# Kernel tuning notes

Measured on AMD Instinct MI355X. Metric: run time of the kernel, lower is better.

The kernel has to match this reference:

```python
import jax, jax.numpy as jnp
import numpy as np

DIM = 1024
N_HEADS = 16
HEAD_DIM = DIM // N_HEADS


def setup_inputs() -> dict:
    key = jax.random.key(0)
    k_x, k_wqkv, k_bqkv, k_wp, k_bp = jax.random.split(key, 5)
    s = 1.0 / np.sqrt(DIM)
    return {
        "x": jax.random.normal(k_x, (2, 2048, DIM), dtype=jnp.float32),
        "w_qkv": jax.random.uniform(k_wqkv, (3 * DIM, DIM), minval=-s, maxval=s, dtype=jnp.float32),
        "b_qkv": jax.random.uniform(k_bqkv, (3 * DIM,), minval=-s, maxval=s, dtype=jnp.float32),
        "w_proj": jax.random.uniform(k_wp, (DIM, DIM), minval=-s, maxval=s, dtype=jnp.float32),
        "b_proj": jax.random.uniform(k_bp, (DIM,), minval=-s, maxval=s, dtype=jnp.float32),
    }


def reference(x, w_qkv, b_qkv, w_proj, b_proj):
    B, S, D = x.shape
    H, Hd = N_HEADS, HEAD_DIM
    scale = jnp.asarray(Hd, x.dtype) ** 0.5
    qkv = x @ w_qkv.T + b_qkv                      # [B, S, 3D]
    q, k, v = jnp.split(qkv, 3, axis=-1)
    # [B, S, D] -> [B, H, S, Hd]
    q = q.reshape(B, S, H, Hd).transpose(0, 2, 1, 3)
    k = k.reshape(B, S, H, Hd).transpose(0, 2, 1, 3)
    v = v.reshape(B, S, H, Hd).transpose(0, 2, 1, 3)
    attn = jnp.einsum("bhqd,bhkd->bhqk", q, k) / scale
    attn = jax.nn.softmax(attn, axis=-1)
    out = jnp.einsum("bhqk,bhkd->bhqd", attn, v)   # [B, H, S, Hd]
    out = out.transpose(0, 2, 1, 3).reshape(B, S, D)
    return out @ w_proj.T + b_proj
```

## Files before the change

kernel.cpp:

```cpp
#include <hip/hip_runtime.h>

typedef __bf16 bf16;
typedef __bf16 bf16x4 __attribute__((ext_vector_type(4)));
typedef __bf16 bf16x8 __attribute__((ext_vector_type(8)));
typedef float f32x4 __attribute__((ext_vector_type(4)));
typedef float f32x16 __attribute__((ext_vector_type(16)));

#define DIMD 1024
#define NHEAD 16
#define HDIM 64
#define BATCH 2
#define SEQ 2048
#define MTOT (BATCH*SEQ)

#define EXP2F(x) __builtin_amdgcn_exp2f(x)

#define OFF_XB (0ull)
#define OFF_OB (0ull)
#define OFF_VT (8ull<<20)
#define OFF_WP (8ull<<20)
#define OFF_WQ (16ull<<20)

__device__ __forceinline__ void g2l16(const void* g, void* l) {
  __builtin_amdgcn_global_load_lds(
      (const __attribute__((address_space(1))) void*)g,
      (__attribute__((address_space(3))) void*)l,
      16, 0, 0);
}

__global__ __launch_bounds__(256) void cvt_kernel(const float* __restrict__ in,
                                                  bf16* __restrict__ out, int n4) {
  int i = blockIdx.x * blockDim.x + threadIdx.x;
  if (i < n4) {
    float4 v = ((const float4*)in)[i];
    bf16x4 o = { (bf16)v.x, (bf16)v.y, (bf16)v.z, (bf16)v.w };
    ((bf16x4*)out)[i] = o;
  }
}

__global__ __launch_bounds__(256) void cvt2_kernel(
    const float* __restrict__ x, const float* __restrict__ wq,
    bf16* __restrict__ xb, bf16* __restrict__ wqb) {
  const int NX = MTOT * DIMD / 4;
  const int NW = 3 * DIMD * DIMD / 4;
  int i = blockIdx.x * blockDim.x + threadIdx.x;
  if (i < NX) {
    float4 v = ((const float4*)x)[i];
    bf16x4 o = { (bf16)v.x, (bf16)v.y, (bf16)v.z, (bf16)v.w };
    ((bf16x4*)xb)[i] = o;
  } else if (i < NX + NW) {
    int j = i - NX;
    float4 v = ((const float4*)wq)[j];
    bf16x4 o = { (bf16)v.x, (bf16)v.y, (bf16)v.z, (bf16)v.w };
    ((bf16x4*)wqb)[j] = o;
  }
}

__global__ __launch_bounds__(256, 3) void gemm_qkv(
    const bf16* __restrict__ A, const bf16* __restrict__ Bt,
    const float* __restrict__ bias,
    bf16* __restrict__ Qb, bf16* __restrict__ Kb, bf16* __restrict__ Vt)
{
  __shared__ bf16 lA[2][128 * 32];
  __shared__ bf16 lB[2][128 * 32];
  const int tid = threadIdx.x;
  const int wave = tid >> 6, lane = tid & 63;
  const int l15 = lane & 15, quad = lane >> 4;
  const int wm = wave >> 1, wn = wave & 1;
  const int tm = blockIdx.y * 128, tn = blockIdx.x * 128;

  f32x4 acc[4][4] = {};

  const int srow = tid >> 2, sch = (tid & 3) * 8;
  const bf16* ga = &A[(size_t)(tm + srow) * DIMD + sch];
  const bf16* gb = &Bt[(size_t)(tn + srow) * DIMD + sch];

  g2l16(ga,                     &lA[0][wave * 512]);
  g2l16(ga + (size_t)64 * DIMD, &lA[0][2048 + wave * 512]);
  g2l16(gb,                     &lB[0][wave * 512]);
  g2l16(gb + (size_t)64 * DIMD, &lB[0][2048 + wave * 512]);

  for (int kt = 0; kt < 32; kt++) {
    __syncthreads();

    if (kt < 31) {
      const int kn = (kt + 1) * 32;
      bf16* nA = lA[(kt + 1) & 1];
      bf16* nB = lB[(kt + 1) & 1];
      g2l16(ga + kn,                     &nA[wave * 512]);
      g2l16(ga + kn + (size_t)64 * DIMD, &nA[2048 + wave * 512]);
      g2l16(gb + kn,                     &nB[wave * 512]);
      g2l16(gb + kn + (size_t)64 * DIMD, &nB[2048 + wave * 512]);
    }

    const bf16* sA = lA[kt & 1];
    const bf16* sB = lB[kt & 1];
    bf16x8 af[4], bfr[4];
#pragma unroll
    for (int i = 0; i < 4; i++)
      af[i] = *(const bf16x8*)&sA[(wm * 64 + i * 16 + l15) * 32 + quad * 8];
#pragma unroll
    for (int i = 0; i < 4; i++)
      bfr[i] = *(const bf16x8*)&sB[(wn * 64 + i * 16 + l15) * 32 + quad * 8];
#pragma unroll
    for (int i = 0; i < 4; i++)
#pragma unroll
      for (int j = 0; j < 4; j++)
        acc[i][j] = __builtin_amdgcn_mfma_f32_16x16x32_bf16(af[i], bfr[j], acc[i][j], 0, 0, 0);
  }

  const int sel = tn >> 10;
#pragma unroll
  for (int j = 0; j < 4; j++) {
    const int n = tn + wn * 64 + j * 16 + l15;
    const float bv = bias[n];
    const int d = n & 1023, h = d >> 6, hd = d & 63;
#pragma unroll
    for (int i = 0; i < 4; i++) {
      const int mbase = tm + wm * 64 + i * 16 + quad * 4;
      const int b = mbase >> 11, s0 = mbase & 2047;
      const int bh = b * NHEAD + h;
      if (sel == 2) {
        bf16x4 vv = { (bf16)(acc[i][j][0] + bv), (bf16)(acc[i][j][1] + bv),
                      (bf16)(acc[i][j][2] + bv), (bf16)(acc[i][j][3] + bv) };
        *(bf16x4*)&Vt[((size_t)bh * HDIM + hd) * SEQ + s0] = vv;
      } else {
#pragma unroll
        for (int r = 0; r < 4; r++) {
          float v = acc[i][j][r] + bv;
          if (sel == 0)
            Qb[((size_t)bh * SEQ + s0 + r) * HDIM + hd] = (bf16)(v * 0.18033688f);
          else
            Kb[((size_t)bh * SEQ + s0 + r) * HDIM + hd] = (bf16)v;
        }
      }
    }
  }
}

__global__ __launch_bounds__(256, 2) void gemm_proj(
    const bf16* __restrict__ A, const bf16* __restrict__ Bt,
    const float* __restrict__ bias, float* __restrict__ out)
{
  __shared__ bf16 lA[2][64 * 32];
  __shared__ bf16 lB[2][128 * 32];
  const int tid = threadIdx.x;
  const int wave = tid >> 6, lane = tid & 63;
  const int l15 = lane & 15, quad = lane >> 4;
  const int tm = blockIdx.y * 64, tn = blockIdx.x * 128;

  f32x4 acc[4][2] = {};

  const int srow = tid >> 2, sch = (tid & 3) * 8;
  const bf16* ga = &A[(size_t)(tm + srow) * DIMD + sch];
  const bf16* gb = &Bt[(size_t)(tn + srow) * DIMD + sch];

  g2l16(ga,                     &lA[0][wave * 512]);
  g2l16(gb,                     &lB[0][wave * 512]);
  g2l16(gb + (size_t)64 * DIMD, &lB[0][2048 + wave * 512]);

  for (int kt = 0; kt < 32; kt++) {
    __syncthreads();

    if (kt < 31) {
      const int kn = (kt + 1) * 32;
      bf16* nA = lA[(kt + 1) & 1];
      bf16* nB = lB[(kt + 1) & 1];
      g2l16(ga + kn,                     &nA[wave * 512]);
      g2l16(gb + kn,                     &nB[wave * 512]);
      g2l16(gb + kn + (size_t)64 * DIMD, &nB[2048 + wave * 512]);
    }

    const bf16* sA = lA[kt & 1];
    const bf16* sB = lB[kt & 1];
    bf16x8 af[4], bfr[2];
#pragma unroll
    for (int i = 0; i < 4; i++)
      af[i] = *(const bf16x8*)&sA[(i * 16 + l15) * 32 + quad * 8];
#pragma unroll
    for (int j = 0; j < 2; j++)
      bfr[j] = *(const bf16x8*)&sB[(wave * 32 + j * 16 + l15) * 32 + quad * 8];
#pragma unroll
    for (int i = 0; i < 4; i++)
#pragma unroll
      for (int j = 0; j < 2; j++)
        acc[i][j] = __builtin_amdgcn_mfma_f32_16x16x32_bf16(af[i], bfr[j], acc[i][j], 0, 0, 0);
  }

#pragma unroll
  for (int j = 0; j < 2; j++) {
    const int n = tn + wave * 32 + j * 16 + l15;
    const float bv = bias[n];
#pragma unroll
    for (int i = 0; i < 4; i++) {
      const int mbase = tm + i * 16 + quad * 4;
#pragma unroll
      for (int r = 0; r < 4; r++)
        out[(size_t)(mbase + r) * DIMD + n] = acc[i][j][r] + bv;
    }
  }
}

#define LSTR 72
__global__ __launch_bounds__(256, 2) void attn_kernel(
    const bf16* __restrict__ Qb, const bf16* __restrict__ Kb,
    const bf16* __restrict__ Vt, bf16* __restrict__ Ob)
{
  __shared__ bf16 lKV[2][2][64 * LSTR];

  const int tid = threadIdx.x;
  const int wave = tid >> 6, lane = tid & 63;
  const int l31 = lane & 31, h = lane >> 5;
  const int xcd = blockIdx.x & 7, grp = blockIdx.x >> 3;
  const int bh = xcd + 8 * (grp & 3);
  const int qt = grp >> 2;

  const int qrow = qt * 128 + wave * 32 + l31;
  const bf16* qp = Qb + ((size_t)bh * SEQ + qrow) * HDIM + h * 8;
  bf16x8 qf[4];
#pragma unroll
  for (int c = 0; c < 4; c++) qf[c] = *(const bf16x8*)(qp + c * 16);

  const int srow = tid >> 3;
  const int sch = (tid & 7) * 8;
  const bf16* kg = Kb + ((size_t)bh * SEQ + srow) * HDIM + sch;
  const bf16* vg = Vt + ((size_t)bh * HDIM + srow) * SEQ + sch;

  uint4 kr0 = *(const uint4*)(kg);
  uint4 kr1 = *(const uint4*)(kg + 32 * HDIM);
  uint4 vr0 = *(const uint4*)(vg);
  uint4 vr1 = *(const uint4*)(vg + 32 * SEQ);

  bf16x8 pf[4];

  f32x16 o0 = {}, o1 = {};
  float mrow = -1e30f, lrow = 0.f;

  for (int kt = 0; kt < SEQ / 64; kt++) {
    bf16* sK = lKV[kt & 1][0];
    bf16* sV = lKV[kt & 1][1];
    *(uint4*)&sK[srow * LSTR + sch]        = kr0;
    *(uint4*)&sK[(32 + srow) * LSTR + sch] = kr1;
    *(uint4*)&sV[srow * LSTR + sch]        = vr0;
    *(uint4*)&sV[(32 + srow) * LSTR + sch] = vr1;
    __syncthreads();

    const int ktn = (kt + 1) & (SEQ / 64 - 1);
    kr0 = *(const uint4*)(kg + (size_t)ktn * 64 * HDIM);
    kr1 = *(const uint4*)(kg + (size_t)ktn * 64 * HDIM + 32 * HDIM);
    vr0 = *(const uint4*)(vg + ktn * 64);
    vr1 = *(const uint4*)(vg + ktn * 64 + 32 * SEQ);

    f32x16 s0 = {}, s1 = {};
#pragma unroll
    for (int c = 0; c < 4; c++) {
      bf16x8 k0 = *(const bf16x8*)&sK[l31 * LSTR + c * 16 + h * 8];
      bf16x8 k1 = *(const bf16x8*)&sK[(32 + l31) * LSTR + c * 16 + h * 8];
      s0 = __builtin_amdgcn_mfma_f32_32x32x16_bf16(k0, qf[c], s0, 0, 0, 0);
      s1 = __builtin_amdgcn_mfma_f32_32x32x16_bf16(k1, qf[c], s1, 0, 0, 0);
    }

    if (kt > 0) {
      const bf16* pV = lKV[(kt + 1) & 1][1];
#pragma unroll
      for (int c = 0; c < 4; c++) {
        bf16x8 v0 = *(const bf16x8*)&pV[l31 * LSTR + c * 16 + h * 8];
        bf16x8 v1 = *(const bf16x8*)&pV[(32 + l31) * LSTR + c * 16 + h * 8];
        o0 = __builtin_amdgcn_mfma_f32_32x32x16_bf16(v0, pf[c], o0, 0, 0, 0);
        o1 = __builtin_amdgcn_mfma_f32_32x32x16_bf16(v1, pf[c], o1, 0, 0, 0);
      }
    }

    float mx = -1e30f;
#pragma unroll
    for (int r = 0; r < 16; r++) { mx = fmaxf(mx, s0[r]); mx = fmaxf(mx, s1[r]); }
    mx = fmaxf(mx, __shfl_xor(mx, 32, 64));
    const float nm = fmaxf(mrow, mx);
    const float alpha = EXP2F(mrow - nm);
    mrow = nm;

    float rs = 0.f;
#pragma unroll
    for (int r = 0; r < 16; r++) {
      const float p0 = EXP2F(s0[r] - nm);
      const float p1 = EXP2F(s1[r] - nm);
      s0[r] = p0; s1[r] = p1;
      rs += p0 + p1;
    }
    rs += __shfl_xor(rs, 32, 64);
    lrow = lrow * alpha + rs;

#pragma unroll
    for (int r = 0; r < 16; r++) { o0[r] *= alpha; o1[r] *= alpha; }

#pragma unroll
    for (int g = 0; g < 2; g++) {
      const f32x16& sg = (g == 0) ? s0 : s1;
#pragma unroll
      for (int cp = 0; cp < 2; cp++) {
        bf16x4 pk0 = { (bf16)sg[8 * cp + 0], (bf16)sg[8 * cp + 1],
                       (bf16)sg[8 * cp + 2], (bf16)sg[8 * cp + 3] };
        bf16x4 pk1 = { (bf16)sg[8 * cp + 4], (bf16)sg[8 * cp + 5],
                       (bf16)sg[8 * cp + 6], (bf16)sg[8 * cp + 7] };
        uint2 w0 = *(uint2*)&pk0;
        uint2 w1 = *(uint2*)&pk1;
        unsigned send0 = h ? w0.x : w1.x;
        unsigned send1 = h ? w0.y : w1.y;
        unsigned recv0 = __shfl_xor(send0, 32, 64);
        unsigned recv1 = __shfl_xor(send1, 32, 64);
        union { unsigned u[4]; bf16x8 v; } f;
        f.u[0] = h ? recv0 : w0.x;
        f.u[1] = h ? recv1 : w0.y;
        f.u[2] = h ? w1.x : recv0;
        f.u[3] = h ? w1.y : recv1;
        pf[2 * g + cp] = f.v;
      }
    }
  }

  {
    const bf16* pV = lKV[1][1];
#pragma unroll
    for (int c = 0; c < 4; c++) {
      bf16x8 v0 = *(const bf16x8*)&pV[l31 * LSTR + c * 16 + h * 8];
      bf16x8 v1 = *(const bf16x8*)&pV[(32 + l31) * LSTR + c * 16 + h * 8];
      o0 = __builtin_amdgcn_mfma_f32_32x32x16_bf16(v0, pf[c], o0, 0, 0, 0);
      o1 = __builtin_amdgcn_mfma_f32_32x32x16_bf16(v1, pf[c], o1, 0, 0, 0);
    }
  }

  const int b = bh >> 4, head = bh & 15;
  const float inv = 1.f / lrow;
  const size_t base = ((size_t)b * SEQ + qrow) * DIMD + head * HDIM;
#pragma unroll
  for (int g = 0; g < 4; g++) {
    bf16x4 oa = { (bf16)(o0[4*g] * inv), (bf16)(o0[4*g+1] * inv),
                  (bf16)(o0[4*g+2] * inv), (bf16)(o0[4*g+3] * inv) };
    bf16x4 ob = { (bf16)(o1[4*g] * inv), (bf16)(o1[4*g+1] * inv),
                  (bf16)(o1[4*g+2] * inv), (bf16)(o1[4*g+3] * inv) };
    *(bf16x4*)&Ob[base + g * 8 + h * 4]      = oa;
    *(bf16x4*)&Ob[base + 32 + g * 8 + h * 4] = ob;
  }
}

extern "C" void kernel_launch(void* const* d_in, const int* in_sizes, int n_in,
                              void* d_out, int out_size, void* d_ws, size_t ws_size,
                              hipStream_t stream) {
  const float* x      = (const float*)d_in[0];
  const float* w_qkv  = (const float*)d_in[1];
  const float* b_qkv  = (const float*)d_in[2];
  const float* w_proj = (const float*)d_in[3];
  const float* b_proj = (const float*)d_in[4];
  float* out = (float*)d_out;
  char* ws = (char*)d_ws;

  bf16* Qb = (bf16*)d_out;
  bf16* Kb = (bf16*)d_out + (size_t)MTOT * DIMD;
  bf16* xb     = (bf16*)(ws + OFF_XB);
  bf16* Ob     = (bf16*)(ws + OFF_OB);
  bf16* Vt     = (bf16*)(ws + OFF_VT);
  bf16* wprojb = (bf16*)(ws + OFF_WP);
  bf16* wqkvb  = (bf16*)(ws + OFF_WQ);

  const int NCVT = (MTOT * DIMD / 4) + (3 * DIMD * DIMD / 4);
  cvt2_kernel<<<NCVT / 256, 256, 0, stream>>>(x, w_qkv, xb, wqkvb);
  gemm_qkv<<<dim3(24, 32), 256, 0, stream>>>(xb, wqkvb, b_qkv, Qb, Kb, Vt);
  attn_kernel<<<BATCH * NHEAD * (SEQ / 128), 256, 0, stream>>>(Qb, Kb, Vt, Ob);
  cvt_kernel<<<(DIMD * DIMD / 4) / 256, 256, 0, stream>>>(w_proj, wprojb, DIMD * DIMD / 4);
  gemm_proj<<<dim3(8, 64), 256, 0, stream>>>(Ob, wprojb, b_proj, out);
}
```

Baseline: 190.1 us.

## Split attention KV sequence into two halves with a separate combine kernel

Runs attention as a split-KV (flash-decoding style) pass: each block handles half of the key sequence, which doubles the grid to 1024 blocks. Each block writes unnormalized fp32 partial outputs plus the row max and sum to workspace. A new combine kernel rescales and merges the two halves and writes bf16 output. This raises parallelism and occupancy across CUs, at the cost of extra fp32 partial traffic, an extra launch, and the Q load and prologue being repeated per half.

```diff
diff --git a/kernel.cpp b/kernel.cpp
--- a/kernel.cpp
+++ b/kernel.cpp
@@ -20,6 +20,8 @@
 #define OFF_VT (8ull<<20)
 #define OFF_WP (8ull<<20)
 #define OFF_WQ (16ull<<20)
+#define OFF_PH (32ull<<20)
+#define OFF_ML (64ull<<20)
 
 __device__ __forceinline__ void g2l16(const void* g, void* l) {
   __builtin_amdgcn_global_load_lds(
@@ -204,16 +206,19 @@
 #define LSTR 72
 __global__ __launch_bounds__(256, 2) void attn_kernel(
     const bf16* __restrict__ Qb, const bf16* __restrict__ Kb,
-    const bf16* __restrict__ Vt, bf16* __restrict__ Ob)
+    const bf16* __restrict__ Vt, float* __restrict__ ph,
+    float* __restrict__ ml)
 {
   __shared__ bf16 lKV[2][2][64 * LSTR];
 
   const int tid = threadIdx.x;
   const int wave = tid >> 6, lane = tid & 63;
   const int l31 = lane & 31, h = lane >> 5;
-  const int xcd = blockIdx.x & 7, grp = blockIdx.x >> 3;
+  const int bid = blockIdx.x;
+  const int xcd = bid & 7, grp = bid >> 3;
   const int bh = xcd + 8 * (grp & 3);
-  const int qt = grp >> 2;
+  const int qt = (grp >> 2) & 15;
+  const int half = grp >> 6;
 
   const int qrow = qt * 128 + wave * 32 + l31;
   const bf16* qp = Qb + ((size_t)bh * SEQ + qrow) * HDIM + h * 8;
@@ -223,8 +228,8 @@
 
   const int srow = tid >> 3;
   const int sch = (tid & 7) * 8;
-  const bf16* kg = Kb + ((size_t)bh * SEQ + srow) * HDIM + sch;
-  const bf16* vg = Vt + ((size_t)bh * HDIM + srow) * SEQ + sch;
+  const bf16* kg = Kb + ((size_t)bh * SEQ + half * 1024 + srow) * HDIM + sch;
+  const bf16* vg = Vt + ((size_t)bh * HDIM + srow) * SEQ + half * 1024 + sch;
 
   uint4 kr0 = *(const uint4*)(kg);
   uint4 kr1 = *(const uint4*)(kg + 32 * HDIM);
@@ -236,7 +241,7 @@
   f32x16 o0 = {}, o1 = {};
   float mrow = -1e30f, lrow = 0.f;
 
-  for (int kt = 0; kt < SEQ / 64; kt++) {
+  for (int kt = 0; kt < 16; kt++) {
     bf16* sK = lKV[kt & 1][0];
     bf16* sV = lKV[kt & 1][1];
     *(uint4*)&sK[srow * LSTR + sch]        = kr0;
@@ -245,7 +250,7 @@
     *(uint4*)&sV[(32 + srow) * LSTR + sch] = vr1;
     __syncthreads();
 
-    const int ktn = (kt + 1) & (SEQ / 64 - 1);
+    const int ktn = (kt + 1) & 15;
     kr0 = *(const uint4*)(kg + (size_t)ktn * 64 * HDIM);
     kr1 = *(const uint4*)(kg + (size_t)ktn * 64 * HDIM + 32 * HDIM);
     vr0 = *(const uint4*)(vg + ktn * 64);
@@ -329,18 +334,46 @@
     }
   }
 
-  const int b = bh >> 4, head = bh & 15;
-  const float inv = 1.f / lrow;
-  const size_t base = ((size_t)b * SEQ + qrow) * DIMD + head * HDIM;
+  const size_t prow = (size_t)(half * 32 + bh) * SEQ + qrow;
+  float* pb = ph + prow * HDIM;
 #pragma unroll
   for (int g = 0; g < 4; g++) {
-    bf16x4 oa = { (bf16)(o0[4*g] * inv), (bf16)(o0[4*g+1] * inv),
-                  (bf16)(o0[4*g+2] * inv), (bf16)(o0[4*g+3] * inv) };
-    bf16x4 ob = { (bf16)(o1[4*g] * inv), (bf16)(o1[4*g+1] * inv),
-                  (bf16)(o1[4*g+2] * inv), (bf16)(o1[4*g+3] * inv) };
-    *(bf16x4*)&Ob[base + g * 8 + h * 4]      = oa;
-    *(bf16x4*)&Ob[base + 32 + g * 8 + h * 4] = ob;
-  }
+    float4 fa = { o0[4*g], o0[4*g+1], o0[4*g+2], o0[4*g+3] };
+    float4 fb = { o1[4*g], o1[4*g+1], o1[4*g+2], o1[4*g+3] };
+    *(float4*)&pb[g * 8 + h * 4]      = fa;
+    *(float4*)&pb[32 + g * 8 + h * 4] = fb;
+  }
+  if (h == 0) {
+    float2 mlv = { mrow, lrow };
+    *(float2*)&ml[prow * 2] = mlv;
+  }
+}
+
+__global__ __launch_bounds__(256) void combine_kernel(
+    const float* __restrict__ ph, const float* __restrict__ ml,
+    bf16* __restrict__ Ob)
+{
+  const int tid = threadIdx.x;
+  const int row = blockIdx.x * 16 + (tid >> 4);
+  const int c = (tid & 15) * 4;
+  const size_t r0 = (size_t)row, r1 = (size_t)(32 * SEQ) * NHEAD / NHEAD * 0 + 65536 + row;
+
+  float2 ml0 = *(const float2*)&ml[r0 * 2];
+  float2 ml1 = *(const float2*)&ml[r1 * 2];
+  const float ms = fmaxf(ml0.x, ml1.x);
+  const float w0 = EXP2F(ml0.x - ms), w1 = EXP2F(ml1.x - ms);
+  const float inv = 1.f / (ml0.y * w0 + ml1.y * w1);
+
+  float4 a = *(const float4*)&ph[r0 * HDIM + c];
+  float4 b = *(const float4*)&ph[r1 * HDIM + c];
+
+  const int bh = row >> 11, s = row & 2047;
+  const int bb = bh >> 4, head = bh & 15;
+  bf16x4 o = { (bf16)((a.x * w0 + b.x * w1) * inv),
+               (bf16)((a.y * w0 + b.y * w1) * inv),
+               (bf16)((a.z * w0 + b.z * w1) * inv),
+               (bf16)((a.w * w0 + b.w * w1) * inv) };
+  *(bf16x4*)&Ob[((size_t)bb * SEQ + s) * DIMD + head * HDIM + c] = o;
 }
 
 extern "C" void kernel_launch(void* const* d_in, const int* in_sizes, int n_in,
@@ -361,11 +394,14 @@
   bf16* Vt     = (bf16*)(ws + OFF_VT);
   bf16* wprojb = (bf16*)(ws + OFF_WP);
   bf16* wqkvb  = (bf16*)(ws + OFF_WQ);
+  float* ph    = (float*)(ws + OFF_PH);
+  float* ml    = (float*)(ws + OFF_ML);
 
   const int NCVT = (MTOT * DIMD / 4) + (3 * DIMD * DIMD / 4);
   cvt2_kernel<<<NCVT / 256, 256, 0, stream>>>(x, w_qkv, xb, wqkvb);
   gemm_qkv<<<dim3(24, 32), 256, 0, stream>>>(xb, wqkvb, b_qkv, Qb, Kb, Vt);
-  attn_kernel<<<BATCH * NHEAD * (SEQ / 128), 256, 0, stream>>>(Qb, Kb, Vt, Ob);
+  attn_kernel<<<2 * BATCH * NHEAD * (SEQ / 128), 256, 0, stream>>>(Qb, Kb, Vt, ph, ml);
+  combine_kernel<<<(BATCH * NHEAD * SEQ) / 16, 256, 0, stream>>>(ph, ml, Ob);
   cvt_kernel<<<(DIMD * DIMD / 4) / 256, 256, 0, stream>>>(w_proj, wprojb, DIMD * DIMD / 4);
   gemm_proj<<<dim3(8, 64), 256, 0, stream>>>(Ob, wprojb, b_proj, out);
 }
```

Measured after the change: 198.5 us. 4.4% more time.
